# Kernel tuning notes

Hardware: AMD Instinct MI355X
Metric: run time of the kernel (lower is better)

## Reference

```python
import jax, jax.numpy as jnp
import numpy as np

DECAY = 0.99
EPS = 1e-05
TEMP = 1.0


def setup_inputs() -> dict:
    key = jax.random.key(0)
    k1, k2, k3 = jax.random.split(key, 3)
    B, T, D, C = 64, 512, 256, 1024
    x = jax.random.normal(k1, (B, T, D), dtype=jnp.float32)
    embed = jax.random.normal(k2, (1, C, D), dtype=jnp.float32)
    embed_avg = jax.random.normal(k3, (1, C, D), dtype=jnp.float32)
    cluster_size = jnp.ones((1, C), dtype=jnp.float32)
    return {"x": x, "embed": embed, "embed_avg": embed_avg, "cluster_size": cluster_size}


def reference(x, embed, embed_avg, cluster_size):
    B, T, D = x.shape
    H, C, _ = embed.shape  # H = num_codebooks = 1
    flatten = x.reshape(H, B * T, D)  # pack_one 'h * d'
    e = jax.lax.stop_gradient(embed)  # learnable_codebook = False

    dist = (2.0 * jnp.einsum('hnd,hcd->hnc', flatten, e)
            - jnp.sum(flatten * flatten, axis=-1, keepdims=True)
            - jnp.sum(e * e, axis=-1)[:, None, :])  # [h, N, C]

    # gumbel_sample: deterministic argmax + straight-through one-hot
    embed_ind = jnp.argmax(dist, axis=-1)  # [h, N]
    probs = jax.nn.softmax(dist / TEMP, axis=-1)
    hard = jax.nn.one_hot(embed_ind, C, dtype=dist.dtype)
    embed_onehot = probs + jax.lax.stop_gradient(hard - probs)  # [h, N, C]

    # quantize via onehot matmul (training path)
    quantize = jnp.einsum('hnc,hcd->hnd', embed_onehot, e).reshape(B, T, D)

    # EMA codebook update
    cs_new = DECAY * cluster_size + (1.0 - DECAY) * embed_onehot.sum(axis=1)  # [h, C]
    embed_sum = jnp.einsum('hnd,hnc->hcd', flatten, embed_onehot)  # [h, C, D]
    ea_new = DECAY * embed_avg + (1.0 - DECAY) * embed_sum
    n = jnp.sum(cs_new, axis=-1, keepdims=True)
    cs_smoothed = (cs_new + EPS) / (n + C * EPS) * n  # laplace smoothing * n
    embed_norm = ea_new / cs_smoothed[..., None]  # new codebook [h, C, D]

    return (quantize, embed_ind.reshape(B, T), embed_norm, cs_new)
```

## Files before the change

kernel.cpp:

```cpp
#include <hip/hip_runtime.h>
#include <cstdint>

#define DECAY 0.99f
#define OMD   0.01f
#define EPSV  1e-5f

constexpr int N_PTS   = 32768;
constexpr int D_DIM   = 256;
constexpr int C_CODES = 1024;
constexpr int NKT     = 12;
constexpr int AP      = 512;
constexpr int BP      = 512;

constexpr int PG = 4;
constexpr int PK = 8;
constexpr int LCAP = 8192;

typedef _Float16 half8  __attribute__((ext_vector_type(8)));
typedef _Float16 half4v __attribute__((ext_vector_type(4)));
typedef float    floatx4 __attribute__((ext_vector_type(4)));

constexpr size_t WS_ENORM = 0;
constexpr size_t WS_PCNT  = 2048;
constexpr size_t WS_CAND  = 8192;
constexpr size_t WS_A16   = WS_CAND + 1048576;
constexpr size_t WS_B16   = WS_A16 + 8388608;
constexpr size_t WS_TOTAL_FLOATS = WS_B16 + 262144;

__device__ __forceinline__ void async_copy16(const void* g, void* s) {
    __builtin_amdgcn_global_load_lds(
        (const __attribute__((address_space(1))) unsigned int*)(uintptr_t)g,
        (__attribute__((address_space(3))) unsigned int*)(uintptr_t)s, 16, 0, 0);
}

__global__ __launch_bounds__(256) void vq_prep(const float* __restrict__ X,
                                               const float* __restrict__ E,
                                               _Float16* __restrict__ A,
                                               _Float16* __restrict__ B,
                                               float* __restrict__ enorm) {
    if (blockIdx.x < 8192) {
        int i = blockIdx.x * 256 + threadIdx.x;
        int n = i >> 6, kq = (i & 63) * 4;
        float4 v = reinterpret_cast<const float4*>(X)[i];
        _Float16 h0 = (_Float16)v.x, h1 = (_Float16)v.y, h2 = (_Float16)v.z, h3 = (_Float16)v.w;
        _Float16 l0 = (_Float16)(v.x - (float)h0), l1 = (_Float16)(v.y - (float)h1);
        _Float16 l2 = (_Float16)(v.z - (float)h2), l3 = (_Float16)(v.w - (float)h3);
        half4v hi = {h0, h1, h2, h3};
        half4v lo = {l0, l1, l2, l3};
        _Float16* row = A + (size_t)n * AP;
        *reinterpret_cast<half4v*>(row + kq)       = hi;
        *reinterpret_cast<half4v*>(row + 256 + kq) = lo;
    } else {
        int i = (blockIdx.x - 8192) * 256 + threadIdx.x;
        int c = i >> 6, kq = (i & 63) * 4;
        float4 v = reinterpret_cast<const float4*>(E)[i];
        _Float16 h0 = (_Float16)v.x, h1 = (_Float16)v.y, h2 = (_Float16)v.z, h3 = (_Float16)v.w;
        _Float16 l0 = (_Float16)(v.x - (float)h0), l1 = (_Float16)(v.y - (float)h1);
        _Float16 l2 = (_Float16)(v.z - (float)h2), l3 = (_Float16)(v.w - (float)h3);
        half4v hi = {h0, h1, h2, h3};
        half4v lo = {l0, l1, l2, l3};
        _Float16* row = B + (size_t)c * BP;
        *reinterpret_cast<half4v*>(row + kq)       = hi;
        *reinterpret_cast<half4v*>(row + 256 + kq) = lo;
        float s = v.x * v.x + v.y * v.y + v.z * v.z + v.w * v.w;
        int lane = threadIdx.x & 63;
#pragma unroll
        for (int off = 32; off > 0; off >>= 1) s += __shfl_down(s, off, 64);
        if (lane == 0) enorm[c] = s;
    }
}

__global__ __launch_bounds__(256) void vq_enorm(const float* __restrict__ E,
                                                float* __restrict__ enorm) {
    int c    = blockIdx.x * 4 + (threadIdx.x >> 6);
    int lane = threadIdx.x & 63;
    float4 v = reinterpret_cast<const float4*>(E)[c * 64 + lane];
    float s  = v.x * v.x + v.y * v.y + v.z * v.z + v.w * v.w;
#pragma unroll
    for (int off = 32; off > 0; off >>= 1) s += __shfl_down(s, off, 64);
    if (lane == 0) enorm[c] = s;
}

__global__ __launch_bounds__(256, 3) void vq_gemm(
    const _Float16* __restrict__ A, const _Float16* __restrict__ B,
    const float* __restrict__ enorm, float2* __restrict__ cand) {
    __shared__ _Float16 As[128 * 64];
    __shared__ _Float16 Bs[128 * 64];

    const int L      = blockIdx.x;
    const int within = L >> 3;
    const int ct     = within & 7;
    const int rt     = (L & 7) | ((within >> 3) << 3);
    const int n0     = rt * 128;
    const int cb0    = ct * 128;

    const int tid = threadIdx.x;
    const int w   = tid >> 6;
    const int l   = tid & 63;

    const int srow = l >> 3;
    const int sq   = (l & 7) ^ srow;

    floatx4 acc[4][4] = {};

    for (int kt = 0; kt < NKT; ++kt) {
        const int ka = ((kt < 8) ? (kt & 3) : (kt - 4)) * 64;
        const int kb = (kt < 4) ? kt * 64 : (kt < 8 ? 256 + (kt - 4) * 64 : (kt - 8) * 64);
        __syncthreads();
#pragma unroll
        for (int t = 0; t < 4; ++t) {
            int rr = w * 32 + t * 8;
            const _Float16* ga = A + (size_t)(n0 + rr + srow) * AP + ka + sq * 8;
            async_copy16(ga, &As[rr * 64]);
            const _Float16* gb = B + (size_t)(cb0 + rr + srow) * BP + kb + sq * 8;
            async_copy16(gb, &Bs[rr * 64]);
        }
        __syncthreads();
#pragma unroll
        for (int kk = 0; kk < 2; ++kk) {
            half8 af[4], bf[4];
            int qa = kk * 4 + (l >> 4);
#pragma unroll
            for (int i = 0; i < 4; ++i) {
                int row  = (w & 1) * 64 + 16 * i + (l & 15);
                af[i] = *reinterpret_cast<const half8*>(&As[row * 64 + (qa ^ (row & 7)) * 8]);
                int crow = (w >> 1) * 64 + 16 * i + (l & 15);
                bf[i] = *reinterpret_cast<const half8*>(&Bs[crow * 64 + (qa ^ (crow & 7)) * 8]);
            }
#pragma unroll
            for (int i = 0; i < 4; ++i)
#pragma unroll
                for (int j = 0; j < 4; ++j)
                    acc[i][j] = __builtin_amdgcn_mfma_f32_16x16x32_f16(af[i], bf[j], acc[i][j], 0, 0, 0);
        }
    }

    const int colbase = cb0 + (w >> 1) * 64 + (l & 15);
    float en[4];
#pragma unroll
    for (int j = 0; j < 4; ++j) en[j] = enorm[colbase + 16 * j];

#pragma unroll
    for (int i = 0; i < 4; ++i) {
#pragma unroll
        for (int reg = 0; reg < 4; ++reg) {
            float bv = -3.4e38f;
            int   bi = 0x7fffffff;
#pragma unroll
            for (int j = 0; j < 4; ++j) {
                float v = 2.0f * acc[i][j][reg] - en[j];
                int   c = colbase + 16 * j;
                if (v > bv || (v == bv && c < bi)) { bv = v; bi = c; }
            }
#pragma unroll
            for (int s = 1; s < 16; s <<= 1) {
                float ov = __shfl_xor(bv, s, 64);
                int   oi = __shfl_xor(bi, s, 64);
                if (ov > bv || (ov == bv && oi < bi)) { bv = ov; bi = oi; }
            }
            if ((l & 15) == 0) {
                int row = n0 + (w & 1) * 64 + 16 * i + (l >> 4) * 4 + reg;
                cand[(size_t)row * 16 + ct * 2 + (w >> 1)] = make_float2(bv, (float)bi);
            }
        }
    }
}

__global__ __launch_bounds__(256) void vq_merge3(
    const float2* __restrict__ cand, const float* __restrict__ E,
    float* __restrict__ quant, float* __restrict__ indout) {
    __shared__ int rowsel[64];
    const int tid = threadIdx.x;
    const int n0  = blockIdx.x * 64;

    if (tid < 64) {
        int r = n0 + tid;
        float bv = -3.4e38f;
        int   bi = 0x7fffffff;
#pragma unroll
        for (int t = 0; t < 16; ++t) {
            float2 cv = cand[(size_t)r * 16 + t];
            int ci = (int)cv.y;
            if (cv.x > bv || (cv.x == bv && ci < bi)) { bv = cv.x; bi = ci; }
        }
        bi &= (C_CODES - 1);
        rowsel[tid] = bi;
        indout[r]   = (float)bi;
    }
    __syncthreads();

    const float4* E4 = reinterpret_cast<const float4*>(E);
    float4*       Q4 = reinterpret_cast<float4*>(quant);
    const int lane = tid & 63;
#pragma unroll
    for (int it = 0; it < 16; ++it) {
        int r   = (tid >> 6) + 4 * it;
        int idx = rowsel[r];
        Q4[(n0 + r) * 64 + lane] = E4[idx * 64 + lane];
    }
}

__global__ __launch_bounds__(256) void vq_part(
    const float* __restrict__ X, const float* __restrict__ indf,
    float* __restrict__ P, int* __restrict__ pcnt) {
    __shared__ int list[LCAP];
    __shared__ int cnt[PK];
    __shared__ int lcnt;
    const int cg = blockIdx.x;
    const int g  = blockIdx.y;
    const int t  = threadIdx.x;
    if (t == 0) lcnt = 0;
    if (t < PK) cnt[t] = 0;
    __syncthreads();

    const float4* I4 = reinterpret_cast<const float4*>(indf);
    float4 v[8];
#pragma unroll
    for (int j = 0; j < 8; ++j)
        v[j] = I4[g * 2048 + j * 256 + t];

#pragma unroll
    for (int j = 0; j < 8; ++j) {
        int base = (g * 2048 + j * 256 + t) * 4;
        int k0 = (int)v[j].x, k1 = (int)v[j].y, k2 = (int)v[j].z, k3 = (int)v[j].w;
        if ((k0 >> 3) == cg) { int p = atomicAdd(&lcnt, 1); atomicAdd(&cnt[k0 & 7], 1); if (p < LCAP) list[p] = ((base + 0) << 3) | (k0 & 7); }
        if ((k1 >> 3) == cg) { int p = atomicAdd(&lcnt, 1); atomicAdd(&cnt[k1 & 7], 1); if (p < LCAP) list[p] = ((base + 1) << 3) | (k1 & 7); }
        if ((k2 >> 3) == cg) { int p = atomicAdd(&lcnt, 1); atomicAdd(&cnt[k2 & 7], 1); if (p < LCAP) list[p] = ((base + 2) << 3) | (k2 & 7); }
        if ((k3 >> 3) == cg) { int p = atomicAdd(&lcnt, 1); atomicAdd(&cnt[k3 & 7], 1); if (p < LCAP) list[p] = ((base + 3) << 3) | (k3 & 7); }
    }
    __syncthreads();

    int m = lcnt; if (m > LCAP) m = LCAP;
    float acc[PK] = {0, 0, 0, 0, 0, 0, 0, 0};
    int r = 0;
    for (; r + 8 <= m; r += 8) {
        int e[8];
        float val[8];
#pragma unroll
        for (int q = 0; q < 8; ++q) e[q] = list[r + q];
#pragma unroll
        for (int q = 0; q < 8; ++q) val[q] = X[(size_t)(e[q] >> 3) * D_DIM + t];
#pragma unroll
        for (int q = 0; q < 8; ++q) {
            int k = e[q] & 7;
#pragma unroll
            for (int kk = 0; kk < PK; ++kk) acc[kk] += (k == kk) ? val[q] : 0.0f;
        }
    }
    for (; r < m; ++r) {
        int e = list[r];
        float val = X[(size_t)(e >> 3) * D_DIM + t];
        int k = e & 7;
#pragma unroll
        for (int kk = 0; kk < PK; ++kk) acc[kk] += (k == kk) ? val : 0.0f;
    }

#pragma unroll
    for (int kk = 0; kk < PK; ++kk)
        P[((size_t)g * C_CODES + cg * PK + kk) * D_DIM + t] = acc[kk];
    if (t < PK) pcnt[g * C_CODES + cg * PK + t] = cnt[t];
}

__global__ __launch_bounds__(256) void vq_comb(
    const float* __restrict__ P, const int* __restrict__ pcnt,
    const float* __restrict__ ea, const float* __restrict__ cs_in,
    float* __restrict__ emb_norm, float* __restrict__ cs_out) {
    __shared__ float red[256];
    const int c = blockIdx.x;
    const int t = threadIdx.x;
    red[t] = cs_in[t] + cs_in[t + 256] + cs_in[t + 512] + cs_in[t + 768];
    __syncthreads();
    for (int st = 128; st > 0; st >>= 1) {
        if (t < st) red[t] += red[t + st];
        __syncthreads();
    }
    const float cssum = red[0];

    float s = 0.0f;
#pragma unroll
    for (int g = 0; g < PG; ++g)
        s += P[((size_t)g * C_CODES + c) * D_DIM + t];
    int total = pcnt[c] + pcnt[C_CODES + c] + pcnt[2 * C_CODES + c] + pcnt[3 * C_CODES + c];
    float cs    = DECAY * cs_in[c] + OMD * (float)total;
    float ntot  = DECAY * cssum + OMD * (float)N_PTS;
    float denom = (cs + EPSV) / (ntot + (float)C_CODES * EPSV) * ntot;
    emb_norm[(size_t)c * D_DIM + t] =
        (DECAY * ea[(size_t)c * D_DIM + t] + OMD * s) / denom;
    if (t == 0) cs_out[c] = cs;
}

__global__ __launch_bounds__(256) void vq_main_fb(
    const float* __restrict__ X, const float* __restrict__ E,
    const float* __restrict__ enorm,
    float* __restrict__ quant, float* __restrict__ indout,
    float* __restrict__ counts, float* __restrict__ esum) {
    constexpr int BN = 64, BC = 64, BK = 32, PADR = 68;
    __shared__ float As[BK * PADR];
    __shared__ float Bs[BK * PADR];
    __shared__ float redv[BN * 16];
    __shared__ int   redi[BN * 16];
    __shared__ int   rowsel[BN];

    const int tid = threadIdx.x;
    const int n0  = blockIdx.x * BN;
    const int tr  = tid >> 4;
    const int tc  = tid & 15;
    const int sr  = tid >> 2;
    const int sk  = tid & 3;

    const float4* X4 = reinterpret_cast<const float4*>(X);
    const float4* E4 = reinterpret_cast<const float4*>(E);

    float best[4];
    int   bidx[4];
#pragma unroll
    for (int i = 0; i < 4; i++) { best[i] = -3.4e38f; bidx[i] = 0; }

    for (int c0 = 0; c0 < C_CODES; c0 += BC) {
        float acc[4][4] = {};
        for (int k0 = 0; k0 < D_DIM; k0 += BK) {
            __syncthreads();
#pragma unroll
            for (int it = 0; it < 2; ++it) {
                int   k4 = sk + 4 * it;
                float4 av = X4[(n0 + sr) * 64 + (k0 >> 2) + k4];
                float4 bv = E4[(c0 + sr) * 64 + (k0 >> 2) + k4];
                int kk = k4 * 4;
                As[(kk + 0) * PADR + sr] = av.x;
                As[(kk + 1) * PADR + sr] = av.y;
                As[(kk + 2) * PADR + sr] = av.z;
                As[(kk + 3) * PADR + sr] = av.w;
                Bs[(kk + 0) * PADR + sr] = bv.x;
                Bs[(kk + 1) * PADR + sr] = bv.y;
                Bs[(kk + 2) * PADR + sr] = bv.z;
                Bs[(kk + 3) * PADR + sr] = bv.w;
            }
            __syncthreads();
#pragma unroll
            for (int k = 0; k < BK; ++k) {
                float4 a = *reinterpret_cast<const float4*>(&As[k * PADR + 4 * tr]);
                float4 b = *reinterpret_cast<const float4*>(&Bs[k * PADR + 4 * tc]);
                acc[0][0] += a.x * b.x; acc[0][1] += a.x * b.y;
                acc[0][2] += a.x * b.z; acc[0][3] += a.x * b.w;
                acc[1][0] += a.y * b.x; acc[1][1] += a.y * b.y;
                acc[1][2] += a.y * b.z; acc[1][3] += a.y * b.w;
                acc[2][0] += a.z * b.x; acc[2][1] += a.z * b.y;
                acc[2][2] += a.z * b.z; acc[2][3] += a.z * b.w;
                acc[3][0] += a.w * b.x; acc[3][1] += a.w * b.y;
                acc[3][2] += a.w * b.z; acc[3][3] += a.w * b.w;
            }
        }
        float4 en = *reinterpret_cast<const float4*>(&enorm[c0 + 4 * tc]);
        float enj[4] = {en.x, en.y, en.z, en.w};
#pragma unroll
        for (int i = 0; i < 4; i++)
#pragma unroll
            for (int j = 0; j < 4; j++) {
                float v = 2.0f * acc[i][j] - enj[j];
                int   c = c0 + 4 * tc + j;
                if (v > best[i]) { best[i] = v; bidx[i] = c; }
            }
    }

    __syncthreads();
#pragma unroll
    for (int i = 0; i < 4; i++) {
        redv[(4 * tr + i) * 16 + tc] = best[i];
        redi[(4 * tr + i) * 16 + tc] = bidx[i];
    }
    __syncthreads();
    if (tid < BN) {
        float bv = redv[tid * 16];
        int   bi = redi[tid * 16];
        for (int t = 1; t < 16; t++) {
            float v  = redv[tid * 16 + t];
            int   id = redi[tid * 16 + t];
            if (v > bv || (v == bv && id < bi)) { bv = v; bi = id; }
        }
        rowsel[tid] = bi;
        indout[n0 + tid] = (float)bi;
        unsafeAtomicAdd(&counts[bi], 1.0f);
    }
    __syncthreads();

    float4*   Q4   = reinterpret_cast<float4*>(quant);
    const int lane = tid & 63;
#pragma unroll
    for (int it = 0; it < 16; ++it) {
        int r   = (tid >> 6) + 4 * it;
        int idx = rowsel[r];
        float4 ev = E4[idx * 64 + lane];
        Q4[(n0 + r) * 64 + lane] = ev;
        float4 xv = X4[(n0 + r) * 64 + lane];
        float* dst = &esum[idx * D_DIM + lane * 4];
        unsafeAtomicAdd(dst + 0, xv.x);
        unsafeAtomicAdd(dst + 1, xv.y);
        unsafeAtomicAdd(dst + 2, xv.z);
        unsafeAtomicAdd(dst + 3, xv.w);
    }
}

__global__ __launch_bounds__(1024) void vq_fin1(const float* __restrict__ cs_in,
                                                const float* __restrict__ counts,
                                                float* __restrict__ cs_out,
                                                float* __restrict__ denom) {
    __shared__ float red[1024];
    int   c  = threadIdx.x;
    float cs = DECAY * cs_in[c] + OMD * counts[c];
    cs_out[c] = cs;
    red[c]    = cs;
    __syncthreads();
    for (int s = 512; s > 0; s >>= 1) {
        if (c < s) red[c] += red[c + s];
        __syncthreads();
    }
    float ntot = red[0];
    denom[c] = (cs + EPSV) / (ntot + (float)C_CODES * EPSV) * ntot;
}

__global__ __launch_bounds__(256) void vq_fin2(const float* __restrict__ ea,
                                               const float* __restrict__ esum,
                                               const float* __restrict__ denom,
                                               float* __restrict__ out) {
    int i = blockIdx.x * 256 + threadIdx.x;
    int c = i >> 6;
    float4 a = reinterpret_cast<const float4*>(ea)[i];
    float4 s = reinterpret_cast<const float4*>(esum)[i];
    float  d = denom[c];
    float4 o;
    o.x = (DECAY * a.x + OMD * s.x) / d;
    o.y = (DECAY * a.y + OMD * s.y) / d;
    o.z = (DECAY * a.z + OMD * s.z) / d;
    o.w = (DECAY * a.w + OMD * s.w) / d;
    reinterpret_cast<float4*>(out)[i] = o;
}

extern "C" void kernel_launch(void* const* d_in, const int* in_sizes, int n_in,
                              void* d_out, int out_size, void* d_ws, size_t ws_size,
                              hipStream_t stream) {
    const float* x            = (const float*)d_in[0];
    const float* embed        = (const float*)d_in[1];
    const float* embed_avg    = (const float*)d_in[2];
    const float* cluster_size = (const float*)d_in[3];

    float* out      = (float*)d_out;
    float* quant    = out;
    float* ind      = out + (size_t)N_PTS * D_DIM;
    float* emb_norm = ind + N_PTS;
    float* cs_out   = emb_norm + (size_t)C_CODES * D_DIM;

    float* ws    = (float*)d_ws;
    float* enorm = ws + WS_ENORM;

    if (ws_size >= WS_TOTAL_FLOATS * sizeof(float)) {
        int*      pcnt  = (int*)(ws + WS_PCNT);
        float2*   cand  = (float2*)(ws + WS_CAND);
        float*    P     = ws + WS_CAND;
        _Float16* A16   = (_Float16*)(ws + WS_A16);
        _Float16* B16   = (_Float16*)(ws + WS_B16);

        vq_prep<<<8448, 256, 0, stream>>>(x, embed, A16, B16, enorm);
        vq_gemm<<<2048, 256, 0, stream>>>(A16, B16, enorm, cand);
        vq_merge3<<<N_PTS / 64, 256, 0, stream>>>(cand, embed, quant, ind);
        vq_part<<<dim3(C_CODES / PK, PG), 256, 0, stream>>>(x, ind, P, pcnt);
        vq_comb<<<C_CODES, 256, 0, stream>>>(P, pcnt, embed_avg, cluster_size,
                                             emb_norm, cs_out);
    } else {
        vq_enorm<<<C_CODES / 4, 256, 0, stream>>>(embed, enorm);
        float* countsf = ws + WS_CAND;
        float* esum    = ws + WS_CAND + 1024;
        float* denom   = ws + WS_A16;
        hipMemsetAsync(countsf, 0, (1024 + (size_t)C_CODES * D_DIM) * sizeof(float), stream);
        vq_main_fb<<<N_PTS / 64, 256, 0, stream>>>(x, embed, enorm, quant, ind, countsf, esum);
        vq_fin1<<<1, 1024, 0, stream>>>(cluster_size, countsf, cs_out, denom);
        vq_fin2<<<(C_CODES * D_DIM / 4) / 256, 256, 0, stream>>>(embed_avg, esum, denom, emb_norm);
    }
}
```

Measured before the change: 225.0 us.

## Screen argmax with hi-only fp16 GEMM, recompute ambiguous rows at split precision

The distance GEMM first runs on the fp16 high parts only, using 4 K-tiles instead of 12. It tracks the best and second-best scores per row. Rows whose margin falls below an error bound built from the x-norm and max e-norm are flagged through an atomic list. Only those rows are recomputed with the full hi/lo split GEMM and patched into the outputs. This cuts most of the tensor-core work but adds two kernels, an atomic counter and a launch-wide early-exit grid, and correctness depends on the error bound being conservative.

```diff
diff --git a/kernel.cpp b/kernel.cpp
--- a/kernel.cpp
+++ b/kernel.cpp
@@ -21,9 +21,13 @@
 typedef float    floatx4 __attribute__((ext_vector_type(4)));
 
 constexpr size_t WS_ENORM = 0;
+constexpr size_t WS_FCNT  = 1024;
 constexpr size_t WS_PCNT  = 2048;
-constexpr size_t WS_CAND  = 8192;
-constexpr size_t WS_A16   = WS_CAND + 1048576;
+constexpr size_t WS_XNORM = 8192;
+constexpr size_t WS_CAND4 = 40960;
+constexpr size_t WS_FLAGR = WS_CAND4 + 2097152;
+constexpr size_t WS_CAND2 = WS_FLAGR + 32768;
+constexpr size_t WS_A16   = WS_CAND2 + 1048576;
 constexpr size_t WS_B16   = WS_A16 + 8388608;
 constexpr size_t WS_TOTAL_FLOATS = WS_B16 + 262144;
 
@@ -37,7 +41,9 @@
                                                const float* __restrict__ E,
                                                _Float16* __restrict__ A,
                                                _Float16* __restrict__ B,
-                                               float* __restrict__ enorm) {
+                                               float* __restrict__ enorm,
+                                               float* __restrict__ xnorm,
+                                               int* __restrict__ fcnt) {
     if (blockIdx.x < 8192) {
         int i = blockIdx.x * 256 + threadIdx.x;
         int n = i >> 6, kq = (i & 63) * 4;
@@ -50,7 +56,13 @@
         _Float16* row = A + (size_t)n * AP;
         *reinterpret_cast<half4v*>(row + kq)       = hi;
         *reinterpret_cast<half4v*>(row + 256 + kq) = lo;
+        float s = v.x * v.x + v.y * v.y + v.z * v.z + v.w * v.w;
+        int lane = threadIdx.x & 63;
+#pragma unroll
+        for (int off = 32; off > 0; off >>= 1) s += __shfl_down(s, off, 64);
+        if (lane == 0) xnorm[n] = s;
     } else {
+        if (blockIdx.x == 8192 && threadIdx.x == 0) *fcnt = 0;
         int i = (blockIdx.x - 8192) * 256 + threadIdx.x;
         int c = i >> 6, kq = (i & 63) * 4;
         float4 v = reinterpret_cast<const float4*>(E)[i];
@@ -81,9 +93,9 @@
     if (lane == 0) enorm[c] = s;
 }
 
-__global__ __launch_bounds__(256, 3) void vq_gemm(
+__global__ __launch_bounds__(256, 2) void vq_gemm1(
     const _Float16* __restrict__ A, const _Float16* __restrict__ B,
-    const float* __restrict__ enorm, float2* __restrict__ cand) {
+    const float* __restrict__ enorm, float4* __restrict__ cand4) {
     __shared__ _Float16 As[128 * 64];
     __shared__ _Float16 Bs[128 * 64];
 
@@ -103,16 +115,15 @@
 
     floatx4 acc[4][4] = {};
 
-    for (int kt = 0; kt < NKT; ++kt) {
-        const int ka = ((kt < 8) ? (kt & 3) : (kt - 4)) * 64;
-        const int kb = (kt < 4) ? kt * 64 : (kt < 8 ? 256 + (kt - 4) * 64 : (kt - 8) * 64);
+    for (int kt = 0; kt < 4; ++kt) {
+        const int k0 = kt * 64;
         __syncthreads();
 #pragma unroll
         for (int t = 0; t < 4; ++t) {
             int rr = w * 32 + t * 8;
-            const _Float16* ga = A + (size_t)(n0 + rr + srow) * AP + ka + sq * 8;
+            const _Float16* ga = A + (size_t)(n0 + rr + srow) * AP + k0 + sq * 8;
             async_copy16(ga, &As[rr * 64]);
-            const _Float16* gb = B + (size_t)(cb0 + rr + srow) * BP + kb + sq * 8;
+            const _Float16* gb = B + (size_t)(cb0 + rr + srow) * BP + k0 + sq * 8;
             async_copy16(gb, &Bs[rr * 64]);
         }
         __syncthreads();
@@ -144,6 +155,156 @@
     for (int i = 0; i < 4; ++i) {
 #pragma unroll
         for (int reg = 0; reg < 4; ++reg) {
+            float bv = -3.4e38f, sv = -3.4e38f;
+            int   bi = 0x7fffffff;
+#pragma unroll
+            for (int j = 0; j < 4; ++j) {
+                float v = 2.0f * acc[i][j][reg] - en[j];
+                int   c = colbase + 16 * j;
+                if (v > bv || (v == bv && c < bi)) { sv = bv; bv = v; bi = c; }
+                else sv = fmaxf(sv, v);
+            }
+#pragma unroll
+            for (int s = 1; s < 16; s <<= 1) {
+                float ov  = __shfl_xor(bv, s, 64);
+                int   oi  = __shfl_xor(bi, s, 64);
+                float osv = __shfl_xor(sv, s, 64);
+                if (ov > bv || (ov == bv && oi < bi)) { sv = fmaxf(bv, osv); bv = ov; bi = oi; }
+                else sv = fmaxf(sv, ov);
+            }
+            if ((l & 15) == 0) {
+                int row = n0 + (w & 1) * 64 + 16 * i + (l >> 4) * 4 + reg;
+                cand4[(size_t)row * 16 + ct * 2 + (w >> 1)] =
+                    make_float4(bv, (float)bi, sv, 0.0f);
+            }
+        }
+    }
+}
+
+__global__ __launch_bounds__(256) void vq_merge3f(
+    const float4* __restrict__ cand4, const float* __restrict__ E,
+    const float* __restrict__ enorm, const float* __restrict__ xnorm,
+    float* __restrict__ quant, float* __restrict__ indout,
+    int* __restrict__ flagrows, int* __restrict__ fcnt) {
+    __shared__ int   rowsel[64];
+    __shared__ float emred[256];
+    const int tid = threadIdx.x;
+    const int n0  = blockIdx.x * 64;
+
+    float em = fmaxf(fmaxf(enorm[tid], enorm[tid + 256]),
+                     fmaxf(enorm[tid + 512], enorm[tid + 768]));
+    emred[tid] = em;
+    __syncthreads();
+    for (int st = 128; st > 0; st >>= 1) {
+        if (tid < st) emred[tid] = fmaxf(emred[tid], emred[tid + st]);
+        __syncthreads();
+    }
+    const float emax = emred[0];
+
+    if (tid < 64) {
+        int r = n0 + tid;
+        float b1 = -3.4e38f, b2 = -3.4e38f;
+        int   i1 = 0x7fffffff;
+#pragma unroll
+        for (int t = 0; t < 16; ++t) {
+            float4 cv = cand4[(size_t)r * 16 + t];
+            int ci = (int)cv.y;
+            if (cv.x > b1 || (cv.x == b1 && ci < i1)) { b2 = fmaxf(b1, cv.z); b1 = cv.x; i1 = ci; }
+            else b2 = fmaxf(b2, cv.x);
+        }
+        i1 &= (C_CODES - 1);
+        rowsel[tid] = i1;
+        indout[r]   = (float)i1;
+        float T = 0.00390625f * sqrtf(xnorm[r] * emax) + 0.5f;
+        if (b1 - b2 <= T) { int p = atomicAdd(fcnt, 1); flagrows[p] = r; }
+    }
+    __syncthreads();
+
+    const float4* E4 = reinterpret_cast<const float4*>(E);
+    float4*       Q4 = reinterpret_cast<float4*>(quant);
+    const int lane = tid & 63;
+#pragma unroll
+    for (int it = 0; it < 16; ++it) {
+        int r   = (tid >> 6) + 4 * it;
+        int idx = rowsel[r];
+        Q4[(n0 + r) * 64 + lane] = E4[idx * 64 + lane];
+    }
+}
+
+__global__ __launch_bounds__(256, 2) void vq_gemm2(
+    const _Float16* __restrict__ A, const _Float16* __restrict__ B,
+    const float* __restrict__ enorm, const int* __restrict__ flagrows,
+    const int* __restrict__ fcnt, float2* __restrict__ cand2) {
+    const int fc = *fcnt;
+
+    const int L      = blockIdx.x;
+    const int within = L >> 3;
+    const int ct     = within & 7;
+    const int rt     = (L & 7) | ((within >> 3) << 3);
+    const int n0     = rt * 128;
+    if (n0 >= fc) return;
+    const int cb0    = ct * 128;
+
+    __shared__ _Float16 As[128 * 64];
+    __shared__ _Float16 Bs[128 * 64];
+
+    const int tid = threadIdx.x;
+    const int w   = tid >> 6;
+    const int l   = tid & 63;
+    const int srow = l >> 3;
+    const int sq   = (l & 7) ^ srow;
+
+    int grow[4];
+#pragma unroll
+    for (int t = 0; t < 4; ++t) {
+        int slot = n0 + w * 32 + t * 8 + srow;
+        int r    = (slot < fc) ? flagrows[slot] : 0;
+        grow[t]  = r & (N_PTS - 1);
+    }
+
+    floatx4 acc[4][4] = {};
+
+    for (int kt = 0; kt < NKT; ++kt) {
+        const int ka = ((kt < 8) ? (kt & 3) : (kt - 4)) * 64;
+        const int kb = (kt < 4) ? kt * 64 : (kt < 8 ? 256 + (kt - 4) * 64 : (kt - 8) * 64);
+        __syncthreads();
+#pragma unroll
+        for (int t = 0; t < 4; ++t) {
+            int rr = w * 32 + t * 8;
+            const _Float16* ga = A + (size_t)grow[t] * AP + ka + sq * 8;
+            async_copy16(ga, &As[rr * 64]);
+            const _Float16* gb = B + (size_t)(cb0 + rr + srow) * BP + kb + sq * 8;
+            async_copy16(gb, &Bs[rr * 64]);
+        }
+        __syncthreads();
+#pragma unroll
+        for (int kk = 0; kk < 2; ++kk) {
+            half8 af[4], bf[4];
+            int qa = kk * 4 + (l >> 4);
+#pragma unroll
+            for (int i = 0; i < 4; ++i) {
+                int row  = (w & 1) * 64 + 16 * i + (l & 15);
+                af[i] = *reinterpret_cast<const half8*>(&As[row * 64 + (qa ^ (row & 7)) * 8]);
+                int crow = (w >> 1) * 64 + 16 * i + (l & 15);
+                bf[i] = *reinterpret_cast<const half8*>(&Bs[crow * 64 + (qa ^ (crow & 7)) * 8]);
+            }
+#pragma unroll
+            for (int i = 0; i < 4; ++i)
+#pragma unroll
+                for (int j = 0; j < 4; ++j)
+                    acc[i][j] = __builtin_amdgcn_mfma_f32_16x16x32_f16(af[i], bf[j], acc[i][j], 0, 0, 0);
+        }
+    }
+
+    const int colbase = cb0 + (w >> 1) * 64 + (l & 15);
+    float en[4];
+#pragma unroll
+    for (int j = 0; j < 4; ++j) en[j] = enorm[colbase + 16 * j];
+
+#pragma unroll
+    for (int i = 0; i < 4; ++i) {
+#pragma unroll
+        for (int reg = 0; reg < 4; ++reg) {
             float bv = -3.4e38f;
             int   bi = 0x7fffffff;
 #pragma unroll
@@ -159,33 +320,45 @@
                 if (ov > bv || (ov == bv && oi < bi)) { bv = ov; bi = oi; }
             }
             if ((l & 15) == 0) {
-                int row = n0 + (w & 1) * 64 + 16 * i + (l >> 4) * 4 + reg;
-                cand[(size_t)row * 16 + ct * 2 + (w >> 1)] = make_float2(bv, (float)bi);
-            }
-        }
-    }
-}
-
-__global__ __launch_bounds__(256) void vq_merge3(
-    const float2* __restrict__ cand, const float* __restrict__ E,
+                int slot = n0 + (w & 1) * 64 + 16 * i + (l >> 4) * 4 + reg;
+                cand2[(size_t)slot * 16 + ct * 2 + (w >> 1)] = make_float2(bv, (float)bi);
+            }
+        }
+    }
+}
+
+__global__ __launch_bounds__(256) void vq_patch(
+    const float2* __restrict__ cand2, const int* __restrict__ flagrows,
+    const int* __restrict__ fcnt, const float* __restrict__ E,
     float* __restrict__ quant, float* __restrict__ indout) {
+    int fc = *fcnt;
+    if (fc > N_PTS) fc = N_PTS;
+    const int s0 = blockIdx.x * 64;
+    if (s0 >= fc) return;
+
     __shared__ int rowsel[64];
+    __shared__ int rowid[64];
     const int tid = threadIdx.x;
-    const int n0  = blockIdx.x * 64;
-
     if (tid < 64) {
-        int r = n0 + tid;
-        float bv = -3.4e38f;
-        int   bi = 0x7fffffff;
-#pragma unroll
-        for (int t = 0; t < 16; ++t) {
-            float2 cv = cand[(size_t)r * 16 + t];
-            int ci = (int)cv.y;
-            if (cv.x > bv || (cv.x == bv && ci < bi)) { bv = cv.x; bi = ci; }
-        }
-        bi &= (C_CODES - 1);
-        rowsel[tid] = bi;
-        indout[r]   = (float)bi;
+        int s = s0 + tid;
+        if (s < fc) {
+            int r = flagrows[s] & (N_PTS - 1);
+            float bv = -3.4e38f;
+            int   bi = 0x7fffffff;
+#pragma unroll
+            for (int t = 0; t < 16; ++t) {
+                float2 cv = cand2[(size_t)s * 16 + t];
+                int ci = (int)cv.y;
+                if (cv.x > bv || (cv.x == bv && ci < bi)) { bv = cv.x; bi = ci; }
+            }
+            bi &= (C_CODES - 1);
+            rowsel[tid] = bi;
+            rowid[tid]  = r;
+            indout[r]   = (float)bi;
+        } else {
+            rowsel[tid] = -1;
+            rowid[tid]  = 0;
+        }
     }
     __syncthreads();
 
@@ -194,9 +367,9 @@
     const int lane = tid & 63;
 #pragma unroll
     for (int it = 0; it < 16; ++it) {
-        int r   = (tid >> 6) + 4 * it;
-        int idx = rowsel[r];
-        Q4[(n0 + r) * 64 + lane] = E4[idx * 64 + lane];
+        int rs  = (tid >> 6) + 4 * it;
+        int idx = rowsel[rs];
+        if (idx >= 0) Q4[(size_t)rowid[rs] * 64 + lane] = E4[idx * 64 + lane];
     }
 }
 
@@ -453,22 +626,29 @@
     float* enorm = ws + WS_ENORM;
 
     if (ws_size >= WS_TOTAL_FLOATS * sizeof(float)) {
+        int*      fcnt  = (int*)(ws + WS_FCNT);
         int*      pcnt  = (int*)(ws + WS_PCNT);
-        float2*   cand  = (float2*)(ws + WS_CAND);
-        float*    P     = ws + WS_CAND;
+        float*    xnorm = ws + WS_XNORM;
+        float4*   cand4 = (float4*)(ws + WS_CAND4);
+        float*    P     = ws + WS_CAND4;
+        int*      flagr = (int*)(ws + WS_FLAGR);
+        float2*   cand2 = (float2*)(ws + WS_CAND2);
         _Float16* A16   = (_Float16*)(ws + WS_A16);
         _Float16* B16   = (_Float16*)(ws + WS_B16);
 
-        vq_prep<<<8448, 256, 0, stream>>>(x, embed, A16, B16, enorm);
-        vq_gemm<<<2048, 256, 0, stream>>>(A16, B16, enorm, cand);
-        vq_merge3<<<N_PTS / 64, 256, 0, stream>>>(cand, embed, quant, ind);
+        vq_prep<<<8448, 256, 0, stream>>>(x, embed, A16, B16, enorm, xnorm, fcnt);
+        vq_gemm1<<<2048, 256, 0, stream>>>(A16, B16, enorm, cand4);
+        vq_merge3f<<<N_PTS / 64, 256, 0, stream>>>(cand4, embed, enorm, xnorm,
+                                                   quant, ind, flagr, fcnt);
+        vq_gemm2<<<2048, 256, 0, stream>>>(A16, B16, enorm, flagr, fcnt, cand2);
+        vq_patch<<<N_PTS / 64, 256, 0, stream>>>(cand2, flagr, fcnt, embed, quant, ind);
         vq_part<<<dim3(C_CODES / PK, PG), 256, 0, stream>>>(x, ind, P, pcnt);
         vq_comb<<<C_CODES, 256, 0, stream>>>(P, pcnt, embed_avg, cluster_size,
                                              emb_norm, cs_out);
     } else {
         vq_enorm<<<C_CODES / 4, 256, 0, stream>>>(embed, enorm);
-        float* countsf = ws + WS_CAND;
-        float* esum    = ws + WS_CAND + 1024;
+        float* countsf = ws + WS_CAND4;
+        float* esum    = ws + WS_CAND4 + 1024;
         float* denom   = ws + WS_A16;
         hipMemsetAsync(countsf, 0, (1024 + (size_t)C_CODES * D_DIM) * sizeof(float), stream);
         vq_main_fb<<<N_PTS / 64, 256, 0, stream>>>(x, embed, enorm, quant, ind, countsf, esum);
```

Result: slower. 229.7 us (+2.1%).
